# Kernel tuning notes

Measured on AMD Instinct MI355X. Metric: run time of the kernel, lower is better.

Reference implementation:

```python
import jax, jax.numpy as jnp
import numpy as np

N_NODES = 50000
N_EDGES = 800000
IN_CH = 512
HID = 128
OUT_CH = 2
N_GRAPHS = 64
EPS = 1e-5


def _gcn_conv(x, src, dst, W, b):
    # GCNConv: out = D^-1/2 (A + I) D^-1/2 (x W) + b  (PyG semantics, self-loops added)
    n = x.shape[0]
    h = x @ W  # [N, H]
    loop = jnp.arange(n)
    src2 = jnp.concatenate([src, loop])
    dst2 = jnp.concatenate([dst, loop])
    deg = jax.ops.segment_sum(jnp.ones_like(dst2, dtype=h.dtype), dst2, num_segments=n)
    dinv = jax.lax.rsqrt(deg)  # deg >= 1 due to self-loops
    norm = dinv[src2] * dinv[dst2]  # [E+N]
    msg = h[src2] * norm[:, None]  # gather + normalize
    out = jax.ops.segment_sum(msg, dst2, num_segments=n)  # scatter-add
    return out + b


def _batchnorm_eval(x, gamma, beta, rm, rv):
    return (x - rm) * jax.lax.rsqrt(rv + EPS) * gamma + beta


def setup_inputs() -> dict:
    key = jax.random.key(0)
    ks = jax.random.split(key, 16)
    x = jax.random.normal(ks[0], (N_NODES, IN_CH), dtype=jnp.float32)
    edge_index = jax.random.randint(ks[1], (2, N_EDGES), 0, N_NODES, dtype=jnp.int64)
    batch = jnp.sort(jax.random.randint(ks[2], (N_NODES,), 0, N_GRAPHS, dtype=jnp.int64))
    s1 = 1.0 / np.sqrt(IN_CH)
    s2 = 1.0 / np.sqrt(HID)
    return {
        'x': x,
        'edge_index': edge_index,
        'batch': batch,
        'W1': jax.random.normal(ks[3], (IN_CH, HID), dtype=jnp.float32) * s1,
        'b1': jnp.zeros((HID,), dtype=jnp.float32),
        'gamma1': jax.random.normal(ks[4], (HID,), dtype=jnp.float32) * 0.1 + 1.0,
        'beta1': jax.random.normal(ks[5], (HID,), dtype=jnp.float32) * 0.1,
        'rm1': jax.random.normal(ks[6], (HID,), dtype=jnp.float32) * 0.1,
        'rv1': jax.random.uniform(ks[7], (HID,), dtype=jnp.float32, minval=0.5, maxval=1.5),
        'W2': jax.random.normal(ks[8], (HID, HID), dtype=jnp.float32) * s2,
        'b2': jnp.zeros((HID,), dtype=jnp.float32),
        'gamma2': jax.random.normal(ks[9], (HID,), dtype=jnp.float32) * 0.1 + 1.0,
        'beta2': jax.random.normal(ks[10], (HID,), dtype=jnp.float32) * 0.1,
        'rm2': jax.random.normal(ks[11], (HID,), dtype=jnp.float32) * 0.1,
        'rv2': jax.random.uniform(ks[12], (HID,), dtype=jnp.float32, minval=0.5, maxval=1.5),
        'Wl': jax.random.normal(ks[13], (HID, OUT_CH), dtype=jnp.float32) * s2,
        'bl': jnp.zeros((OUT_CH,), dtype=jnp.float32),
    }


def reference(x, edge_index, batch, W1, b1, gamma1, beta1, rm1, rv1,
              W2, b2, gamma2, beta2, rm2, rv2, Wl, bl):
    # Eval mode: BatchNorm uses running stats; dropout is identity.
    src, dst = edge_index[0], edge_index[1]
    h = _gcn_conv(x, src, dst, W1, b1)
    h = jax.nn.relu(_batchnorm_eval(h, gamma1, beta1, rm1, rv1))
    h = _gcn_conv(h, src, dst, W2, b2)
    h = jax.nn.relu(_batchnorm_eval(h, gamma2, beta2, rm2, rv2))
    # global mean pool over graphs in the batch
    sums = jax.ops.segment_sum(h, batch, num_segments=N_GRAPHS)  # [G, H]
    counts = jax.ops.segment_sum(jnp.ones((h.shape[0],), dtype=h.dtype), batch, num_segments=N_GRAPHS)
    pooled = sums / jnp.maximum(counts, 1.0)[:, None]
    return pooled @ Wl + bl  # [G, OUT_CH]
```

## Files before the change

### kernel.cpp

```cpp
#include <hip/hip_runtime.h>

#define EPSV 1e-5f

typedef __attribute__((ext_vector_type(8))) short short8;
typedef __attribute__((ext_vector_type(4))) float f32x4;
typedef unsigned int uint;

__global__ __launch_bounds__(256) void init_k(int* __restrict__ cnt, int nnodes) {
    int i = blockIdx.x * 256 + threadIdx.x;
    if (i < nnodes) cnt[i] = 0;
}

__global__ __launch_bounds__(128) void gstart_k(const int* __restrict__ batch,
                                                int* __restrict__ gstart,
                                                int nnodes, int ngraphs) {
    int g = threadIdx.x;
    if (g > ngraphs) return;
    int lo = 0, hi = nnodes;
    while (lo < hi) {
        int mid = (lo + hi) >> 1;
        if (batch[mid] < g) lo = mid + 1; else hi = mid;
    }
    gstart[g] = lo;
}

__global__ __launch_bounds__(256) void degcount_k(const int* __restrict__ dst,
                                                  int* __restrict__ cnt,
                                                  int nedges) {
    int i = blockIdx.x * 256 + threadIdx.x;
    if (i < nedges) atomicAdd(&cnt[dst[i]], 1);
}

__global__ __launch_bounds__(256) void dinv_k(const int* __restrict__ cnt,
                                              float* __restrict__ dinv, int nnodes) {
    int i = blockIdx.x * 256 + threadIdx.x;
    if (i < nnodes) dinv[i] = rsqrtf(1.0f + (float)cnt[i]);
}

__global__ __launch_bounds__(256) void scan1_k(const int* __restrict__ cnt,
                                               int* __restrict__ rowptr,
                                               int* __restrict__ bsum, int n) {
    __shared__ int sh[256];
    const int tx = threadIdx.x;
    const int base = blockIdx.x * 1024;
    int v[4];
    int s = 0;
#pragma unroll
    for (int j = 0; j < 4; j++) {
        int idx = base + tx * 4 + j;
        v[j] = (idx < n) ? cnt[idx] : 0;
        s += v[j];
    }
    sh[tx] = s;
    __syncthreads();
#pragma unroll
    for (int off = 1; off < 256; off <<= 1) {
        int t = (tx >= off) ? sh[tx - off] : 0;
        __syncthreads();
        sh[tx] += t;
        __syncthreads();
    }
    int run = sh[tx] - s;
#pragma unroll
    for (int j = 0; j < 4; j++) {
        int idx = base + tx * 4 + j;
        if (idx < n) rowptr[idx] = run;
        run += v[j];
    }
    if (tx == 255) bsum[blockIdx.x] = sh[255];
}

__global__ __launch_bounds__(64) void scan2_k(int* __restrict__ bsum, int nb) {
    __shared__ int sh[64];
    const int tx = threadIdx.x;
    int v = (tx < nb) ? bsum[tx] : 0;
    sh[tx] = v;
    __syncthreads();
#pragma unroll
    for (int off = 1; off < 64; off <<= 1) {
        int t = (tx >= off) ? sh[tx - off] : 0;
        __syncthreads();
        sh[tx] += t;
        __syncthreads();
    }
    if (tx < nb) bsum[tx] = sh[tx] - v;
}

__global__ __launch_bounds__(256) void scan3_k(int* __restrict__ rowptr,
                                               int* __restrict__ cur,
                                               const int* __restrict__ bsum,
                                               int n, int nedges) {
    const int tx = threadIdx.x;
    const int base = blockIdx.x * 1024;
    int off = bsum[blockIdx.x];
#pragma unroll
    for (int j = 0; j < 4; j++) {
        int idx = base + tx * 4 + j;
        if (idx < n) {
            int r = rowptr[idx] + off;
            rowptr[idx] = r;
            cur[idx] = r;
        }
    }
    if (blockIdx.x == 0 && tx == 0) rowptr[n] = nedges;
}

__global__ __launch_bounds__(256) void fill_k(const int* __restrict__ src,
                                              const int* __restrict__ dst,
                                              int* __restrict__ cur,
                                              int* __restrict__ esrc, int nedges) {
    int i = blockIdx.x * 256 + threadIdx.x;
    if (i >= nedges) return;
    int pos = atomicAdd(&cur[dst[i]], 1);
    esrc[pos] = src[i];
}

template <int K>
__global__ __launch_bounds__(256) void wprep_k(const float* __restrict__ W,
                                               unsigned short* __restrict__ wThi,
                                               unsigned short* __restrict__ wTlo) {
    int i = blockIdx.x * 256 + threadIdx.x;
    if (i >= K * 128) return;
    int k = i >> 7, c = i & 127;
    float x = W[i];
    unsigned u = __builtin_bit_cast(unsigned, x);
    unsigned short hi = (unsigned short)(u >> 16);
    float hif = __builtin_bit_cast(float, u & 0xffff0000u);
    float lof = x - hif;
    unsigned short lo = (unsigned short)(__builtin_bit_cast(unsigned, lof) >> 16);
    wThi[c * K + k] = hi;
    wTlo[c * K + k] = lo;
}

template <int K>
__global__ __launch_bounds__(256) void gemm_mfma_k(const float* __restrict__ X,
                                                   const unsigned short* __restrict__ wThi,
                                                   const unsigned short* __restrict__ wTlo,
                                                   float* __restrict__ H, int nrows) {
    __shared__ unsigned short bsm[2][128][40];

    const int tx = threadIdx.x;
    const int wave = tx >> 6;
    const int l = tx & 63;
    const int lrow = l & 15;
    const int kgrp = l >> 4;
    const int row0 = blockIdx.x * 64 + wave * 16;

    int arow = row0 + lrow;
    if (arow >= nrows) arow = nrows - 1;
    const float* xrow = X + (size_t)arow * K + kgrp * 8;

    f32x4 acc[8];
#pragma unroll
    for (int g = 0; g < 8; g++) acc[g] = (f32x4){0.f, 0.f, 0.f, 0.f};

    for (int k0 = 0; k0 < K; k0 += 32) {
        __syncthreads();
#pragma unroll
        for (int r = 0; r < 4; r++) {
            int chunk = tx + r * 256;
            int hilo = chunk >> 9;
            int c = (chunk >> 2) & 127;
            int kc = (chunk & 3) * 8;
            const unsigned short* gsrc = (hilo ? wTlo : wThi) + (size_t)c * K + k0 + kc;
            short8 v = *reinterpret_cast<const short8*>(gsrc);
            *reinterpret_cast<short8*>(&bsm[hilo][c][kc]) = v;
        }
        __syncthreads();

        f32x4 x0 = *reinterpret_cast<const f32x4*>(xrow + k0);
        f32x4 x1 = *reinterpret_cast<const f32x4*>(xrow + k0 + 4);
        short8 ah, al;
#pragma unroll
        for (int j = 0; j < 8; j++) {
            float f = (j < 4) ? x0[j] : x1[j - 4];
            unsigned u = __builtin_bit_cast(unsigned, f);
            ah[j] = (short)(u >> 16);
            float hif = __builtin_bit_cast(float, u & 0xffff0000u);
            float lof = f - hif;
            al[j] = (short)(__builtin_bit_cast(unsigned, lof) >> 16);
        }

#pragma unroll
        for (int g = 0; g < 8; g++) {
            short8 bh = *reinterpret_cast<const short8*>(&bsm[0][g * 16 + lrow][kgrp * 8]);
            short8 bl = *reinterpret_cast<const short8*>(&bsm[1][g * 16 + lrow][kgrp * 8]);
            acc[g] = __builtin_amdgcn_mfma_f32_16x16x32_bf16(ah, bh, acc[g], 0, 0, 0);
            acc[g] = __builtin_amdgcn_mfma_f32_16x16x32_bf16(al, bh, acc[g], 0, 0, 0);
            acc[g] = __builtin_amdgcn_mfma_f32_16x16x32_bf16(ah, bl, acc[g], 0, 0, 0);
        }
    }

#pragma unroll
    for (int r = 0; r < 4; r++) {
        int row = row0 + kgrp * 4 + r;
        if (row < nrows) {
            float* hrow = H + (size_t)row * 128 + lrow;
#pragma unroll
            for (int g = 0; g < 8; g++) hrow[g * 16] = acc[g][r];
        }
    }
}

__global__ __launch_bounds__(256) void scale_k(const float* __restrict__ H,
                                               const float* __restrict__ dinv,
                                               uint* __restrict__ hb, int nfeat4) {
    int i = blockIdx.x * 256 + threadIdx.x;
    if (i >= nfeat4) return;
    float dn = dinv[i >> 5];
    f32x4 v = *reinterpret_cast<const f32x4*>(H + (size_t)i * 4);
    uint b[4];
#pragma unroll
    for (int j = 0; j < 4; j++) {
        unsigned u = __builtin_bit_cast(unsigned, v[j] * dn);
        b[j] = u + 0x7fffu + ((u >> 16) & 1u);
    }
    uint2 o;
    o.x = (b[0] >> 16) | (b[1] & 0xffff0000u);
    o.y = (b[2] >> 16) | (b[3] & 0xffff0000u);
    *reinterpret_cast<uint2*>(hb + (size_t)i * 2) = o;
}

__global__ __launch_bounds__(256) void agg_k(const float* __restrict__ H,
                                             const uint* __restrict__ hb,
                                             const int* __restrict__ rowptr,
                                             const int* __restrict__ esrc,
                                             const float* __restrict__ dinv,
                                             const float* __restrict__ bias,
                                             const float* __restrict__ gamma,
                                             const float* __restrict__ beta,
                                             const float* __restrict__ rm,
                                             const float* __restrict__ rv,
                                             float* __restrict__ OUT,
                                             int nnodes) {
    int node = blockIdx.x * 4 + (threadIdx.x >> 6);
    if (node >= nnodes) return;
    node = __builtin_amdgcn_readfirstlane(node);
    const int l = threadIdx.x & 63;
    const int c = l * 2;
    const float dn = dinv[node];
    const int beg = rowptr[node], end = rowptr[node + 1];

    float2 hv = *reinterpret_cast<const float2*>(H + (size_t)node * 128 + c);
    float ax0 = hv.x * dn, ay0 = hv.y * dn;
    float ax1 = 0.f, ay1 = 0.f, ax2 = 0.f, ay2 = 0.f, ax3 = 0.f, ay3 = 0.f;
    const uint* hbl = hb + l;

    int j = beg;
    for (; j + 3 < end; j += 4) {
        int s0 = esrc[j], s1 = esrc[j + 1], s2 = esrc[j + 2], s3 = esrc[j + 3];
        uint u0 = hbl[(size_t)s0 * 64];
        uint u1 = hbl[(size_t)s1 * 64];
        uint u2 = hbl[(size_t)s2 * 64];
        uint u3 = hbl[(size_t)s3 * 64];
        ax0 += __builtin_bit_cast(float, u0 << 16);
        ay0 += __builtin_bit_cast(float, u0 & 0xffff0000u);
        ax1 += __builtin_bit_cast(float, u1 << 16);
        ay1 += __builtin_bit_cast(float, u1 & 0xffff0000u);
        ax2 += __builtin_bit_cast(float, u2 << 16);
        ay2 += __builtin_bit_cast(float, u2 & 0xffff0000u);
        ax3 += __builtin_bit_cast(float, u3 << 16);
        ay3 += __builtin_bit_cast(float, u3 & 0xffff0000u);
    }
    for (; j < end; j++) {
        uint u0 = hbl[(size_t)esrc[j] * 64];
        ax0 += __builtin_bit_cast(float, u0 << 16);
        ay0 += __builtin_bit_cast(float, u0 & 0xffff0000u);
    }
    float accx = (ax0 + ax1) + (ax2 + ax3);
    float accy = (ay0 + ay1) + (ay2 + ay3);

    float v0 = accx * dn + bias[c];
    float v1 = accy * dn + bias[c + 1];
    v0 = (v0 - rm[c])     * rsqrtf(rv[c] + EPSV)     * gamma[c]     + beta[c];
    v1 = (v1 - rm[c + 1]) * rsqrtf(rv[c + 1] + EPSV) * gamma[c + 1] + beta[c + 1];
    v0 = fmaxf(v0, 0.0f);
    v1 = fmaxf(v1, 0.0f);

    *reinterpret_cast<float2*>(OUT + (size_t)node * 128 + c) = make_float2(v0, v1);
}

__global__ __launch_bounds__(256) void pool1_k(const float* __restrict__ V,
                                               const int* __restrict__ gstart,
                                               float* __restrict__ partial) {
    __shared__ float sh[256];
    const int g = blockIdx.x >> 5;
    const int p = blockIdx.x & 31;
    const int tx = threadIdx.x;
    const int ch = tx & 127;
    const int sub = tx >> 7;
    const int beg = gstart[g], end = gstart[g + 1];
    const int chunk = (end - beg + 31) >> 5;
    const int s = beg + p * chunk;
    const int e = min(s + chunk, end);
    float acc = 0.0f;
    for (int i = s + sub; i < e; i += 2)
        acc += V[(size_t)i * 128 + ch];
    sh[tx] = acc;
    __syncthreads();
    if (tx < 128)
        partial[(size_t)blockIdx.x * 128 + tx] = sh[tx] + sh[tx + 128];
}

__global__ __launch_bounds__(128) void pool2_k(const float* __restrict__ partial,
                                               const int* __restrict__ gstart,
                                               float* __restrict__ pooled) {
    const int g = blockIdx.x;
    const int ch = threadIdx.x;
    float s = 0.0f;
#pragma unroll
    for (int p = 0; p < 32; p++)
        s += partial[(size_t)((g << 5) + p) * 128 + ch];
    float cnt = fmaxf((float)(gstart[g + 1] - gstart[g]), 1.0f);
    pooled[g * 128 + ch] = s / cnt;
}

__global__ __launch_bounds__(128) void final_k(const float* __restrict__ pooled,
                                               const float* __restrict__ Wl,
                                               const float* __restrict__ bl,
                                               float* __restrict__ out) {
    int tx = threadIdx.x;
    int g = tx >> 1, o = tx & 1;
    float s = 0.0f;
#pragma unroll 8
    for (int c = 0; c < 128; c++) s += pooled[g * 128 + c] * Wl[c * 2 + o];
    out[tx] = s + bl[o];
}

extern "C" void kernel_launch(void* const* d_in, const int* in_sizes, int n_in,
                              void* d_out, int out_size, void* d_ws, size_t ws_size,
                              hipStream_t stream) {
    const float* x      = (const float*)d_in[0];
    const int*   ei     = (const int*)d_in[1];
    const int*   batch  = (const int*)d_in[2];
    const float* W1     = (const float*)d_in[3];
    const float* b1     = (const float*)d_in[4];
    const float* gamma1 = (const float*)d_in[5];
    const float* beta1  = (const float*)d_in[6];
    const float* rm1    = (const float*)d_in[7];
    const float* rv1    = (const float*)d_in[8];
    const float* W2     = (const float*)d_in[9];
    const float* b2     = (const float*)d_in[10];
    const float* gamma2 = (const float*)d_in[11];
    const float* beta2  = (const float*)d_in[12];
    const float* rm2    = (const float*)d_in[13];
    const float* rv2    = (const float*)d_in[14];
    const float* Wl     = (const float*)d_in[15];
    const float* bl     = (const float*)d_in[16];
    float* out = (float*)d_out;

    const int nnodes  = in_sizes[2];
    const int nedges  = in_sizes[1] / 2;
    const int ngraphs = 64;
    const int* srcp = ei;
    const int* dstp = ei + nedges;

    float* wsA     = (float*)d_ws;
    float* wsB     = wsA + (size_t)nnodes * 128;
    float* dinv    = wsB + (size_t)nnodes * 128;
    float* pooled  = dinv + nnodes;
    float* partial = pooled + 64 * 128;
    int*   cnt     = (int*)(partial + 64 * 32 * 128);
    int*   rowptr  = cnt + nnodes;
    int*   cur     = rowptr + nnodes + 1;
    int*   bsum    = cur + nnodes;
    int*   gstart  = bsum + 64;
    int*   esrc    = gstart + 65;
    uintptr_t wp   = ((uintptr_t)(esrc + nedges) + 15) & ~(uintptr_t)15;
    unsigned short* wt1hi = (unsigned short*)wp;
    unsigned short* wt1lo = wt1hi + 512 * 128;
    unsigned short* wt2hi = wt1lo + 512 * 128;
    unsigned short* wt2lo = wt2hi + 128 * 128;
    uint* hb = (uint*)(wt2lo + 128 * 128);

    dim3 blk(256);
    const int gNodes = (nnodes + 255) / 256;
    const int gEdges = (nedges + 255) / 256;
    const int gGemm  = (nnodes + 63) / 64;
    const int gAgg   = (nnodes + 3) / 4;
    const int nScanB = (nnodes + 1023) / 1024;
    const int nfeat4 = nnodes * 32;
    const int gScale = (nfeat4 + 255) / 256;

    init_k<<<gNodes, blk, 0, stream>>>(cnt, nnodes);
    gstart_k<<<1, 128, 0, stream>>>(batch, gstart, nnodes, ngraphs);
    wprep_k<512><<<(512 * 128) / 256, blk, 0, stream>>>(W1, wt1hi, wt1lo);
    wprep_k<128><<<(128 * 128) / 256, blk, 0, stream>>>(W2, wt2hi, wt2lo);
    degcount_k<<<gEdges, blk, 0, stream>>>(dstp, cnt, nedges);
    dinv_k<<<gNodes, blk, 0, stream>>>(cnt, dinv, nnodes);
    scan1_k<<<nScanB, blk, 0, stream>>>(cnt, rowptr, bsum, nnodes);
    scan2_k<<<1, 64, 0, stream>>>(bsum, nScanB);
    scan3_k<<<nScanB, blk, 0, stream>>>(rowptr, cur, bsum, nnodes, nedges);
    fill_k<<<gEdges, blk, 0, stream>>>(srcp, dstp, cur, esrc, nedges);

    gemm_mfma_k<512><<<gGemm, blk, 0, stream>>>(x, wt1hi, wt1lo, wsA, nnodes);
    scale_k<<<gScale, blk, 0, stream>>>(wsA, dinv, hb, nfeat4);
    agg_k<<<gAgg, blk, 0, stream>>>(wsA, hb, rowptr, esrc, dinv, b1, gamma1, beta1,
                                    rm1, rv1, wsB, nnodes);

    gemm_mfma_k<128><<<gGemm, blk, 0, stream>>>(wsB, wt2hi, wt2lo, wsA, nnodes);
    scale_k<<<gScale, blk, 0, stream>>>(wsA, dinv, hb, nfeat4);
    agg_k<<<gAgg, blk, 0, stream>>>(wsA, hb, rowptr, esrc, dinv, b2, gamma2, beta2,
                                    rm2, rv2, wsB, nnodes);

    pool1_k<<<ngraphs * 32, blk, 0, stream>>>(wsB, gstart, partial);
    pool2_k<<<ngraphs, 128, 0, stream>>>(partial, gstart, pooled);
    final_k<<<1, 128, 0, stream>>>(pooled, Wl, bl, out);
}
```

Before: 287.7 us.

## Double-buffer GEMM weight tiles via direct global-to-LDS loads and fuse scaling epilogue

The GEMM now stages weight tiles into LDS with global_load_lds, double-buffered with an XOR swizzle so the next k-slice loads while MFMAs run on the current one. X rows are also prefetched one iteration ahead. The separate scale kernel is removed. The GEMM epilogue now writes the dinv-scaled bf16 copy directly, which saves a launch and a full reread of H. This adds LDS layout complexity and relies on the swizzle and sync ordering being correct.

```diff
diff --git a/kernel.cpp b/kernel.cpp
--- a/kernel.cpp
+++ b/kernel.cpp
@@ -5,6 +5,7 @@
 typedef __attribute__((ext_vector_type(8))) short short8;
 typedef __attribute__((ext_vector_type(4))) float f32x4;
 typedef unsigned int uint;
+typedef unsigned short ushort;
 
 __global__ __launch_bounds__(256) void init_k(int* __restrict__ cnt, int nnodes) {
     int i = blockIdx.x * 256 + threadIdx.x;
@@ -117,34 +118,46 @@
 
 template <int K>
 __global__ __launch_bounds__(256) void wprep_k(const float* __restrict__ W,
-                                               unsigned short* __restrict__ wThi,
-                                               unsigned short* __restrict__ wTlo) {
+                                               ushort* __restrict__ wThi,
+                                               ushort* __restrict__ wTlo) {
     int i = blockIdx.x * 256 + threadIdx.x;
     if (i >= K * 128) return;
     int k = i >> 7, c = i & 127;
     float x = W[i];
     unsigned u = __builtin_bit_cast(unsigned, x);
-    unsigned short hi = (unsigned short)(u >> 16);
+    ushort hi = (ushort)(u >> 16);
     float hif = __builtin_bit_cast(float, u & 0xffff0000u);
     float lof = x - hif;
-    unsigned short lo = (unsigned short)(__builtin_bit_cast(unsigned, lof) >> 16);
+    ushort lo = (ushort)(__builtin_bit_cast(unsigned, lof) >> 16);
     wThi[c * K + k] = hi;
     wTlo[c * K + k] = lo;
 }
 
 template <int K>
 __global__ __launch_bounds__(256) void gemm_mfma_k(const float* __restrict__ X,
-                                                   const unsigned short* __restrict__ wThi,
-                                                   const unsigned short* __restrict__ wTlo,
-                                                   float* __restrict__ H, int nrows) {
-    __shared__ unsigned short bsm[2][128][40];
+                                                   const ushort* __restrict__ wThi,
+                                                   const ushort* __restrict__ wTlo,
+                                                   const float* __restrict__ dinv,
+                                                   float* __restrict__ H,
+                                                   ushort* __restrict__ hb16,
+                                                   int nrows) {
+    __shared__ ushort bsm[2][8192];
 
     const int tx = threadIdx.x;
-    const int wave = tx >> 6;
+    const int wu = __builtin_amdgcn_readfirstlane(tx >> 6);
     const int l = tx & 63;
     const int lrow = l & 15;
     const int kgrp = l >> 4;
-    const int row0 = blockIdx.x * 64 + wave * 16;
+    const int row0 = blockIdx.x * 64 + wu * 16;
+
+    const ushort* sp[4];
+#pragma unroll
+    for (int q = 0; q < 4; q++) {
+        int chunk = (wu * 4 + q) * 64 + l;
+        int c = chunk >> 3;
+        int sl = (chunk & 7) ^ (c & 7);
+        sp[q] = ((sl >> 2) ? wTlo : wThi) + (size_t)c * K + (sl & 3) * 8;
+    }
 
     int arow = row0 + lrow;
     if (arow >= nrows) arow = nrows - 1;
@@ -154,26 +167,37 @@
 #pragma unroll
     for (int g = 0; g < 8; g++) acc[g] = (f32x4){0.f, 0.f, 0.f, 0.f};
 
-    for (int k0 = 0; k0 < K; k0 += 32) {
-        __syncthreads();
-#pragma unroll
-        for (int r = 0; r < 4; r++) {
-            int chunk = tx + r * 256;
-            int hilo = chunk >> 9;
-            int c = (chunk >> 2) & 127;
-            int kc = (chunk & 3) * 8;
-            const unsigned short* gsrc = (hilo ? wTlo : wThi) + (size_t)c * K + k0 + kc;
-            short8 v = *reinterpret_cast<const short8*>(gsrc);
-            *reinterpret_cast<short8*>(&bsm[hilo][c][kc]) = v;
-        }
-        __syncthreads();
-
-        f32x4 x0 = *reinterpret_cast<const f32x4*>(xrow + k0);
-        f32x4 x1 = *reinterpret_cast<const f32x4*>(xrow + k0 + 4);
+    auto STAGE = [&](int buf, int k0) {
+#pragma unroll
+        for (int q = 0; q < 4; q++) {
+            const ushort* src = sp[q] + k0;
+            ushort* dst = &bsm[buf][(wu * 4 + q) * 512];
+            __builtin_amdgcn_global_load_lds(
+                (const __attribute__((address_space(1))) unsigned int*)(const void*)src,
+                (__attribute__((address_space(3))) unsigned int*)(void*)dst,
+                16, 0, 0);
+        }
+    };
+
+    constexpr int NIT = K / 32;
+    STAGE(0, 0);
+    f32x4 xa = *reinterpret_cast<const f32x4*>(xrow);
+    f32x4 xb = *reinterpret_cast<const f32x4*>(xrow + 4);
+    __syncthreads();
+
+    for (int i = 0; i < NIT; i++) {
+        const int cur = i & 1;
+        if (i + 1 < NIT) STAGE(cur ^ 1, (i + 1) * 32);
+        f32x4 na = xa, nb = xb;
+        if (i + 1 < NIT) {
+            na = *reinterpret_cast<const f32x4*>(xrow + (i + 1) * 32);
+            nb = *reinterpret_cast<const f32x4*>(xrow + (i + 1) * 32 + 4);
+        }
+
         short8 ah, al;
 #pragma unroll
         for (int j = 0; j < 8; j++) {
-            float f = (j < 4) ? x0[j] : x1[j - 4];
+            float f = (j < 4) ? xa[j] : xb[j - 4];
             unsigned u = __builtin_bit_cast(unsigned, f);
             ah[j] = (short)(u >> 16);
             float hif = __builtin_bit_cast(float, u & 0xffff0000u);
@@ -181,44 +205,37 @@
             al[j] = (short)(__builtin_bit_cast(unsigned, lof) >> 16);
         }
 
+        const ushort* b = bsm[cur];
 #pragma unroll
         for (int g = 0; g < 8; g++) {
-            short8 bh = *reinterpret_cast<const short8*>(&bsm[0][g * 16 + lrow][kgrp * 8]);
-            short8 bl = *reinterpret_cast<const short8*>(&bsm[1][g * 16 + lrow][kgrp * 8]);
+            int c = g * 16 + lrow;
+            int sw = c & 7;
+            short8 bh = *reinterpret_cast<const short8*>(&b[c * 64 + ((kgrp ^ sw) * 8)]);
+            short8 bl = *reinterpret_cast<const short8*>(&b[c * 64 + (((4 | kgrp) ^ sw) * 8)]);
             acc[g] = __builtin_amdgcn_mfma_f32_16x16x32_bf16(ah, bh, acc[g], 0, 0, 0);
             acc[g] = __builtin_amdgcn_mfma_f32_16x16x32_bf16(al, bh, acc[g], 0, 0, 0);
             acc[g] = __builtin_amdgcn_mfma_f32_16x16x32_bf16(ah, bl, acc[g], 0, 0, 0);
         }
+        __syncthreads();
+        xa = na; xb = nb;
     }
 
 #pragma unroll
     for (int r = 0; r < 4; r++) {
         int row = row0 + kgrp * 4 + r;
         if (row < nrows) {
+            float dn = dinv[row];
             float* hrow = H + (size_t)row * 128 + lrow;
-#pragma unroll
-            for (int g = 0; g < 8; g++) hrow[g * 16] = acc[g][r];
-        }
-    }
-}
-
-__global__ __launch_bounds__(256) void scale_k(const float* __restrict__ H,
-                                               const float* __restrict__ dinv,
-                                               uint* __restrict__ hb, int nfeat4) {
-    int i = blockIdx.x * 256 + threadIdx.x;
-    if (i >= nfeat4) return;
-    float dn = dinv[i >> 5];
-    f32x4 v = *reinterpret_cast<const f32x4*>(H + (size_t)i * 4);
-    uint b[4];
-#pragma unroll
-    for (int j = 0; j < 4; j++) {
-        unsigned u = __builtin_bit_cast(unsigned, v[j] * dn);
-        b[j] = u + 0x7fffu + ((u >> 16) & 1u);
-    }
-    uint2 o;
-    o.x = (b[0] >> 16) | (b[1] & 0xffff0000u);
-    o.y = (b[2] >> 16) | (b[3] & 0xffff0000u);
-    *reinterpret_cast<uint2*>(hb + (size_t)i * 2) = o;
+            ushort* hbrow = hb16 + (size_t)row * 128 + lrow;
+#pragma unroll
+            for (int g = 0; g < 8; g++) {
+                float v = acc[g][r];
+                hrow[g * 16] = v;
+                unsigned u = __builtin_bit_cast(unsigned, v * dn);
+                hbrow[g * 16] = (ushort)((u + 0x7fffu + ((u >> 16) & 1u)) >> 16);
+            }
+        }
+    }
 }
 
 __global__ __launch_bounds__(256) void agg_k(const float* __restrict__ H,
@@ -367,11 +384,12 @@
     int*   gstart  = bsum + 64;
     int*   esrc    = gstart + 65;
     uintptr_t wp   = ((uintptr_t)(esrc + nedges) + 15) & ~(uintptr_t)15;
-    unsigned short* wt1hi = (unsigned short*)wp;
-    unsigned short* wt1lo = wt1hi + 512 * 128;
-    unsigned short* wt2hi = wt1lo + 512 * 128;
-    unsigned short* wt2lo = wt2hi + 128 * 128;
-    uint* hb = (uint*)(wt2lo + 128 * 128);
+    ushort* wt1hi = (ushort*)wp;
+    ushort* wt1lo = wt1hi + 512 * 128;
+    ushort* wt2hi = wt1lo + 512 * 128;
+    ushort* wt2lo = wt2hi + 128 * 128;
+    ushort* hb16  = (ushort*)(wt2lo + 128 * 128);
+    uint*   hb    = (uint*)hb16;
 
     dim3 blk(256);
     const int gNodes = (nnodes + 255) / 256;
@@ -379,8 +397,6 @@
     const int gGemm  = (nnodes + 63) / 64;
     const int gAgg   = (nnodes + 3) / 4;
     const int nScanB = (nnodes + 1023) / 1024;
-    const int nfeat4 = nnodes * 32;
-    const int gScale = (nfeat4 + 255) / 256;
 
     init_k<<<gNodes, blk, 0, stream>>>(cnt, nnodes);
     gstart_k<<<1, 128, 0, stream>>>(batch, gstart, nnodes, ngraphs);
@@ -393,13 +409,11 @@
     scan3_k<<<nScanB, blk, 0, stream>>>(rowptr, cur, bsum, nnodes, nedges);
     fill_k<<<gEdges, blk, 0, stream>>>(srcp, dstp, cur, esrc, nedges);
 
-    gemm_mfma_k<512><<<gGemm, blk, 0, stream>>>(x, wt1hi, wt1lo, wsA, nnodes);
-    scale_k<<<gScale, blk, 0, stream>>>(wsA, dinv, hb, nfeat4);
+    gemm_mfma_k<512><<<gGemm, blk, 0, stream>>>(x, wt1hi, wt1lo, dinv, wsA, hb16, nnodes);
     agg_k<<<gAgg, blk, 0, stream>>>(wsA, hb, rowptr, esrc, dinv, b1, gamma1, beta1,
                                     rm1, rv1, wsB, nnodes);
 
-    gemm_mfma_k<128><<<gGemm, blk, 0, stream>>>(wsB, wt2hi, wt2lo, wsA, nnodes);
-    scale_k<<<gScale, blk, 0, stream>>>(wsA, dinv, hb, nfeat4);
+    gemm_mfma_k<128><<<gGemm, blk, 0, stream>>>(wsB, wt2hi, wt2lo, dinv, wsA, hb16, nnodes);
     agg_k<<<gAgg, blk, 0, stream>>>(wsA, hb, rowptr, esrc, dinv, b2, gamma2, beta2,
                                     rm2, rv2, wsB, nnodes);
 
```

Measured after the change: 280.3 us. 2.6% less time.
